# Optimization experiments

Hardware: AMD Instinct MI355X
Metric: run time of the kernel (lower is better)

The kernel has to match this reference:

```python
import jax, jax.numpy as jnp
import numpy as np

DIM = 64  # QK head dim, matches init kwarg 'dim'

def setup_inputs() -> dict:
    key = jax.random.key(0)
    kq, kk, kv = jax.random.split(key, 3)
    B, L, C, D, H = 2, 2048, 16, DIM, 64
    query = jax.random.normal(kq, (B, L, C, D), dtype=jnp.float32)
    k_ = jax.random.normal(kk, (B, L, C, D), dtype=jnp.float32)
    value = jax.random.normal(kv, (B, L, C, H), dtype=jnp.float32)
    return {"query": query, "key": k_, "value": value}

def reference(query, key, value):
    scaler = 1.0 / jnp.sqrt(jnp.float32(DIM))
    # score: [b, c, l, m]
    score = jnp.einsum('blcd,bmcd->bclm', query, key) * scaler
    # mask=False, dropout=0 -> identity
    attn = jax.nn.softmax(score, axis=3)
    # out: [b, l, c, h]
    out = jnp.einsum('bmch,bclm->blch', value, attn)
    return out
```

## Files before the change

### kernel.cpp

```cpp
#include <hip/hip_runtime.h>
#include <hip/hip_bf16.h>
#include <stdint.h>

#define B_ 2
#define L_ 2048
#define C_ 16
#define D_ 64
#define H_ 64
#define QBLK 128
#define KVBLK 64
#define NTILES 32
#define NTHREADS 256
#define NHEADS 32
#define TILE_ELEMS 4096
#define TENSOR_ELEMS (NHEADS * NTILES * TILE_ELEMS)

typedef __attribute__((ext_vector_type(8))) short bf16x8;
typedef __attribute__((ext_vector_type(16))) float f32x16;
typedef __attribute__((ext_vector_type(8))) unsigned short u16x8;

__device__ inline unsigned short f2bf(float f) {
  union { float f; unsigned int u; } v; v.f = f;
  unsigned int u = v.u;
  unsigned int r = (u + 0x7FFFu + ((u >> 16) & 1u)) >> 16;
  return (unsigned short)r;
}

__device__ inline float fast_exp2(float x) {
#if __has_builtin(__builtin_amdgcn_exp2f)
  return __builtin_amdgcn_exp2f(x);
#else
  return exp2f(x);
#endif
}

__device__ inline void gload_lds16(const unsigned short* g, unsigned short* l) {
  __builtin_amdgcn_global_load_lds(
      (const __attribute__((address_space(1))) unsigned int*)g,
      (__attribute__((address_space(3))) unsigned int*)l, 16, 0, 0);
}

__device__ inline unsigned cvt_pk_bf16(float lo, float hi) {
  unsigned r;
  asm("v_cvt_pk_bf16_f32 %0, %1, %2" : "=v"(r) : "v"(lo), "v"(hi));
  return r;
}

__device__ inline void pl32swap(unsigned &x, unsigned &y) {
#if __has_builtin(__builtin_amdgcn_permlane32_swap)
  auto r = __builtin_amdgcn_permlane32_swap(x, y, false, false);
  x = r[0]; y = r[1];
#else
  asm("v_permlane32_swap_b32 %0, %1" : "+v"(x), "+&v"(y));
#endif
}

__device__ inline float xmax32(float v) {
  unsigned x = __float_as_uint(v), y = x;
  pl32swap(x, y);
  return fmaxf(__uint_as_float(x), __uint_as_float(y));
}

__device__ inline float xsum32(float v) {
  unsigned x = __float_as_uint(v), y = x;
  pl32swap(x, y);
  return __uint_as_float(x) + __uint_as_float(y);
}

#define SLOT(grp, row) ((grp) ^ ((row) & 7) ^ (((row) & 8) >> 1))

__global__ __launch_bounds__(256) void prepack_kernel(
    const float* __restrict__ Kg, const float* __restrict__ Vg,
    unsigned short* __restrict__ Kb, unsigned short* __restrict__ Vb) {
  int idx = blockIdx.x * 256 + threadIdx.x;
  if (idx < 524288) {
    int i = idx;
    int grp = i & 7, row = (i >> 3) & 63, t = (i >> 9) & 31, head = i >> 14;
    int b = head >> 4, c = head & 15;
    const float* src = Kg + ((size_t)(b * L_ + t * 64 + row) * C_ + c) * D_ + grp * 8;
    float4 a0 = ((const float4*)src)[0];
    float4 a1 = ((const float4*)src)[1];
    u16x8 pk;
    pk[0] = f2bf(a0.x); pk[1] = f2bf(a0.y); pk[2] = f2bf(a0.z); pk[3] = f2bf(a0.w);
    pk[4] = f2bf(a1.x); pk[5] = f2bf(a1.y); pk[6] = f2bf(a1.z); pk[7] = f2bf(a1.w);
    size_t dst = ((size_t)(head * 32 + t) * 64 + row) * 64 + SLOT(grp, row) * 8;
    *(u16x8*)&Kb[dst] = pk;
  } else {
    int i = idx - 524288;
    int h = i & 63, grp = (i >> 6) & 7, t = (i >> 9) & 31, head = i >> 14;
    int b = head >> 4, c = head & 15;
    const float* src = Vg + ((size_t)(b * L_ + t * 64 + grp * 8) * C_ + c) * H_ + h;
    u16x8 pv;
#pragma unroll
    for (int j = 0; j < 8; ++j) pv[j] = f2bf(src[(size_t)j * C_ * H_]);
    size_t dst = ((size_t)(head * 32 + t) * 64 + h) * 64 + SLOT(grp, h) * 8;
    *(u16x8*)&Vb[dst] = pv;
  }
}

__global__ __launch_bounds__(NTHREADS, 2) void attn_fwd_kernel(
    const float* __restrict__ Qg,
    const unsigned short* __restrict__ Kb,
    const unsigned short* __restrict__ Vb,
    float* __restrict__ Og) {
  __shared__ unsigned short Ks2[3][TILE_ELEMS];
  __shared__ unsigned short Vt2[3][TILE_ELEMS];

  const int tid  = threadIdx.x;
  const int lane = tid & 63;
  const int w    = tid >> 6;
  const int ql   = lane & 31;
  const int u    = lane >> 5;

  const int bid   = blockIdx.x;
  const int swz   = (bid & 7) * 64 + (bid >> 3);
  const int head  = swz >> 4;
  const int qtile = swz & 15;
  const int b     = head >> 4;
  const int c     = head & 15;
  const int q0    = qtile * QBLK;

  const unsigned short* KbH = Kb + (size_t)head * NTILES * TILE_ELEMS;
  const unsigned short* VbH = Vb + (size_t)head * NTILES * TILE_ELEMS;

  const int qr = q0 + w * 32 + ql;
  const float* qrow = Qg + ((size_t)(b * L_ + qr) * C_ + c) * D_;
  bf16x8 qf[4];
#pragma unroll
  for (int ks = 0; ks < 4; ++ks) {
    float4 a0 = *(const float4*)(qrow + ks * 16 + u * 8);
    float4 a1 = *(const float4*)(qrow + ks * 16 + u * 8 + 4);
    bf16x8 q8;
    q8[0] = (short)f2bf(a0.x); q8[1] = (short)f2bf(a0.y);
    q8[2] = (short)f2bf(a0.z); q8[3] = (short)f2bf(a0.w);
    q8[4] = (short)f2bf(a1.x); q8[5] = (short)f2bf(a1.y);
    q8[6] = (short)f2bf(a1.z); q8[7] = (short)f2bf(a1.w);
    qf[ks] = q8;
  }

  f32x16 o0, o1;
#pragma unroll
  for (int i = 0; i < 16; ++i) { o0[i] = 0.f; o1[i] = 0.f; }
  float m_i = -1e30f, l_i = 0.f;
  const float sc2 = 0.125f * 1.44269504088896340736f;

  gload_lds16(KbH + tid * 8, &Ks2[0][tid * 8]);
  gload_lds16(KbH + 2048 + tid * 8, &Ks2[0][2048 + tid * 8]);
  gload_lds16(VbH + tid * 8, &Vt2[0][tid * 8]);
  gload_lds16(VbH + 2048 + tid * 8, &Vt2[0][2048 + tid * 8]);
  gload_lds16(KbH + TILE_ELEMS + tid * 8, &Ks2[1][tid * 8]);
  gload_lds16(KbH + TILE_ELEMS + 2048 + tid * 8, &Ks2[1][2048 + tid * 8]);
  gload_lds16(VbH + TILE_ELEMS + tid * 8, &Vt2[1][tid * 8]);
  gload_lds16(VbH + TILE_ELEMS + 2048 + tid * 8, &Vt2[1][2048 + tid * 8]);
  asm volatile("s_waitcnt vmcnt(4)" ::: "memory");
  __builtin_amdgcn_s_barrier();
  __builtin_amdgcn_sched_barrier(0);

  int cur = 0, stg = 2;
  for (int t = 0; t < NTILES; ++t) {
    {
      const int tl = (t + 2 < NTILES) ? (t + 2) : (NTILES - 1);
      const size_t toff = (size_t)tl * TILE_ELEMS + tid * 8;
      gload_lds16(KbH + toff, &Ks2[stg][tid * 8]);
      gload_lds16(KbH + toff + 2048, &Ks2[stg][2048 + tid * 8]);
      gload_lds16(VbH + toff, &Vt2[stg][tid * 8]);
      gload_lds16(VbH + toff + 2048, &Vt2[stg][2048 + tid * 8]);
    }

    const unsigned short* KsB = Ks2[cur];
    const unsigned short* VtB = Vt2[cur];

    f32x16 s0, s1;
#pragma unroll
    for (int i = 0; i < 16; ++i) { s0[i] = 0.f; s1[i] = 0.f; }
    __builtin_amdgcn_s_setprio(1);
#pragma unroll
    for (int ks = 0; ks < 4; ++ks) {
      const int col8 = 2 * ks + u;
      const int sw = SLOT(col8, ql) * 8;
      const bf16x8 ka0 = *(const bf16x8*)&KsB[ql * 64 + sw];
      const bf16x8 ka1 = *(const bf16x8*)&KsB[(32 + ql) * 64 + sw];
      s0 = __builtin_amdgcn_mfma_f32_32x32x16_bf16(ka0, qf[ks], s0, 0, 0, 0);
      s1 = __builtin_amdgcn_mfma_f32_32x32x16_bf16(ka1, qf[ks], s1, 0, 0, 0);
    }
    __builtin_amdgcn_s_setprio(0);

    float a8[8];
#pragma unroll
    for (int i = 0; i < 8; ++i)
      a8[i] = fmaxf(fmaxf(s0[i], s0[i + 8]), fmaxf(s1[i], s1[i + 8]));
    float b4a = fmaxf(a8[0], a8[1]), b4b = fmaxf(a8[2], a8[3]);
    float b4c = fmaxf(a8[4], a8[5]), b4d = fmaxf(a8[6], a8[7]);
    float rm = fmaxf(fmaxf(b4a, b4b), fmaxf(b4c, b4d));
    rm = xmax32(rm);
    const float rmx = rm * sc2;
    if (__any(rmx > m_i + 8.f)) {
      float mn = fmaxf(m_i, rmx);
      float so = fast_exp2(m_i - mn);
      m_i = mn;
#pragma unroll
      for (int i = 0; i < 16; ++i) { o0[i] *= so; o1[i] *= so; }
      l_i *= so;
    }

    float rst[4];
    bf16x8 pf[4];
#pragma unroll
    for (int tq = 0; tq < 4; ++tq) {
      const int be = ((2 * tq) & 3) * 4;
      const int bo = ((2 * tq + 1) & 3) * 4;
      float p0[4], p1[4];
#pragma unroll
      for (int r = 0; r < 4; ++r) {
        float se = (tq < 2) ? s0[be + r] : s1[be + r];
        float so_ = (tq < 2) ? s0[bo + r] : s1[bo + r];
        p0[r] = fast_exp2(__builtin_fmaf(se, sc2, -m_i));
        p1[r] = fast_exp2(__builtin_fmaf(so_, sc2, -m_i));
      }
      rst[tq] = ((p0[0] + p0[1]) + (p0[2] + p0[3])) +
                ((p1[0] + p1[1]) + (p1[2] + p1[3]));
      unsigned x0 = cvt_pk_bf16(p0[0], p0[1]);
      unsigned x1 = cvt_pk_bf16(p0[2], p0[3]);
      unsigned y0 = cvt_pk_bf16(p1[0], p1[1]);
      unsigned y1 = cvt_pk_bf16(p1[2], p1[3]);
      pl32swap(x0, y0);
      pl32swap(x1, y1);
      union { unsigned wd[4]; bf16x8 v; } pk;
      pk.wd[0] = x0; pk.wd[1] = x1; pk.wd[2] = y0; pk.wd[3] = y1;
      pf[tq] = pk.v;
    }
    l_i += xsum32((rst[0] + rst[1]) + (rst[2] + rst[3]));

    __builtin_amdgcn_s_setprio(1);
#pragma unroll
    for (int m = 0; m < 4; ++m) {
      const int col8 = 2 * m + u;
      const int sw = SLOT(col8, ql) * 8;
      const bf16x8 va0 = *(const bf16x8*)&VtB[ql * 64 + sw];
      const bf16x8 va1 = *(const bf16x8*)&VtB[(32 + ql) * 64 + sw];
      o0 = __builtin_amdgcn_mfma_f32_32x32x16_bf16(va0, pf[m], o0, 0, 0, 0);
      o1 = __builtin_amdgcn_mfma_f32_32x32x16_bf16(va1, pf[m], o1, 0, 0, 0);
    }
    __builtin_amdgcn_s_setprio(0);

    __builtin_amdgcn_sched_barrier(0);
    asm volatile("s_waitcnt vmcnt(4) lgkmcnt(0)" ::: "memory");
    __builtin_amdgcn_s_barrier();
    __builtin_amdgcn_sched_barrier(0);

    cur = (cur == 2) ? 0 : cur + 1;
    stg = (stg == 2) ? 0 : stg + 1;
  }

  const float inv = 1.0f / l_i;
  float* orow = Og + ((size_t)(b * L_ + qr) * C_ + c) * H_;
#pragma unroll
  for (int rg = 0; rg < 4; ++rg) {
    float4 v0, v1;
    v0.x = o0[rg * 4 + 0] * inv; v0.y = o0[rg * 4 + 1] * inv;
    v0.z = o0[rg * 4 + 2] * inv; v0.w = o0[rg * 4 + 3] * inv;
    v1.x = o1[rg * 4 + 0] * inv; v1.y = o1[rg * 4 + 1] * inv;
    v1.z = o1[rg * 4 + 2] * inv; v1.w = o1[rg * 4 + 3] * inv;
    *(float4*)(orow + 8 * rg + 4 * u) = v0;
    *(float4*)(orow + 32 + 8 * rg + 4 * u) = v1;
  }
}

extern "C" void kernel_launch(void* const* d_in, const int* in_sizes, int n_in,
                              void* d_out, int out_size, void* d_ws, size_t ws_size,
                              hipStream_t stream) {
  const float* Qg = (const float*)d_in[0];
  const float* Kg = (const float*)d_in[1];
  const float* Vg = (const float*)d_in[2];
  float* Og = (float*)d_out;

  unsigned short* Kb = (unsigned short*)d_ws;
  unsigned short* Vb = Kb + (size_t)TENSOR_ELEMS;

  prepack_kernel<<<4096, 256, 0, stream>>>(Kg, Vg, Kb, Vb);

  dim3 grid(NHEADS * (L_ / QBLK));
  dim3 block(NTHREADS);
  attn_fwd_kernel<<<grid, block, 0, stream>>>(Qg, Kb, Vb, Og);
}
```

Before: 69.04 us.

## Process two 32-row query groups per wave to double K/V tile reuse

Doubles the query block from 128 to 256 rows so that each wave handles two 32-row query groups. Each K and V fragment read from LDS feeds four MFMAs instead of two, and the grid halves to 256 blocks. This cuts K/V global and LDS traffic per query. In exchange, register pressure roughly doubles, so launch bounds drop to one block per SIMD group, and the smaller grid may underfill the 256 CUs.

```diff
diff --git a/kernel.cpp b/kernel.cpp
--- a/kernel.cpp
+++ b/kernel.cpp
@@ -7,7 +7,7 @@
 #define C_ 16
 #define D_ 64
 #define H_ 64
-#define QBLK 128
+#define QBLK 256
 #define KVBLK 64
 #define NTILES 32
 #define NTHREADS 256
@@ -98,7 +98,7 @@
   }
 }
 
-__global__ __launch_bounds__(NTHREADS, 2) void attn_fwd_kernel(
+__global__ __launch_bounds__(NTHREADS, 1) void attn_fwd_kernel(
     const float* __restrict__ Qg,
     const unsigned short* __restrict__ Kb,
     const unsigned short* __restrict__ Vb,
@@ -113,9 +113,9 @@
   const int u    = lane >> 5;
 
   const int bid   = blockIdx.x;
-  const int swz   = (bid & 7) * 64 + (bid >> 3);
-  const int head  = swz >> 4;
-  const int qtile = swz & 15;
+  const int swz   = (bid & 7) * 32 + (bid >> 3);
+  const int head  = swz >> 3;
+  const int qtile = swz & 7;
   const int b     = head >> 4;
   const int c     = head & 15;
   const int q0    = qtile * QBLK;
@@ -123,25 +123,33 @@
   const unsigned short* KbH = Kb + (size_t)head * NTILES * TILE_ELEMS;
   const unsigned short* VbH = Vb + (size_t)head * NTILES * TILE_ELEMS;
 
-  const int qr = q0 + w * 32 + ql;
-  const float* qrow = Qg + ((size_t)(b * L_ + qr) * C_ + c) * D_;
-  bf16x8 qf[4];
-#pragma unroll
-  for (int ks = 0; ks < 4; ++ks) {
-    float4 a0 = *(const float4*)(qrow + ks * 16 + u * 8);
-    float4 a1 = *(const float4*)(qrow + ks * 16 + u * 8 + 4);
-    bf16x8 q8;
-    q8[0] = (short)f2bf(a0.x); q8[1] = (short)f2bf(a0.y);
-    q8[2] = (short)f2bf(a0.z); q8[3] = (short)f2bf(a0.w);
-    q8[4] = (short)f2bf(a1.x); q8[5] = (short)f2bf(a1.y);
-    q8[6] = (short)f2bf(a1.z); q8[7] = (short)f2bf(a1.w);
-    qf[ks] = q8;
+  bf16x8 qf[2][4];
+#pragma unroll
+  for (int g = 0; g < 2; ++g) {
+    const int qr = q0 + w * 64 + g * 32 + ql;
+    const float* qrow = Qg + ((size_t)(b * L_ + qr) * C_ + c) * D_;
+#pragma unroll
+    for (int ks = 0; ks < 4; ++ks) {
+      float4 a0 = *(const float4*)(qrow + ks * 16 + u * 8);
+      float4 a1 = *(const float4*)(qrow + ks * 16 + u * 8 + 4);
+      bf16x8 q8;
+      q8[0] = (short)f2bf(a0.x); q8[1] = (short)f2bf(a0.y);
+      q8[2] = (short)f2bf(a0.z); q8[3] = (short)f2bf(a0.w);
+      q8[4] = (short)f2bf(a1.x); q8[5] = (short)f2bf(a1.y);
+      q8[6] = (short)f2bf(a1.z); q8[7] = (short)f2bf(a1.w);
+      qf[g][ks] = q8;
+    }
   }
 
-  f32x16 o0, o1;
-#pragma unroll
-  for (int i = 0; i < 16; ++i) { o0[i] = 0.f; o1[i] = 0.f; }
-  float m_i = -1e30f, l_i = 0.f;
+  f32x16 o[2][2];
+#pragma unroll
+  for (int g = 0; g < 2; ++g)
+#pragma unroll
+    for (int hb = 0; hb < 2; ++hb)
+#pragma unroll
+      for (int i = 0; i < 16; ++i) o[g][hb][i] = 0.f;
+  float m_i[2] = {-1e30f, -1e30f};
+  float l_i[2] = {0.f, 0.f};
   const float sc2 = 0.125f * 1.44269504088896340736f;
 
   gload_lds16(KbH + tid * 8, &Ks2[0][tid * 8]);
@@ -170,9 +178,13 @@
     const unsigned short* KsB = Ks2[cur];
     const unsigned short* VtB = Vt2[cur];
 
-    f32x16 s0, s1;
-#pragma unroll
-    for (int i = 0; i < 16; ++i) { s0[i] = 0.f; s1[i] = 0.f; }
+    f32x16 s[2][2];
+#pragma unroll
+    for (int g = 0; g < 2; ++g)
+#pragma unroll
+      for (int hf = 0; hf < 2; ++hf)
+#pragma unroll
+        for (int i = 0; i < 16; ++i) s[g][hf][i] = 0.f;
     __builtin_amdgcn_s_setprio(1);
 #pragma unroll
     for (int ks = 0; ks < 4; ++ks) {
@@ -180,56 +192,62 @@
       const int sw = SLOT(col8, ql) * 8;
       const bf16x8 ka0 = *(const bf16x8*)&KsB[ql * 64 + sw];
       const bf16x8 ka1 = *(const bf16x8*)&KsB[(32 + ql) * 64 + sw];
-      s0 = __builtin_amdgcn_mfma_f32_32x32x16_bf16(ka0, qf[ks], s0, 0, 0, 0);
-      s1 = __builtin_amdgcn_mfma_f32_32x32x16_bf16(ka1, qf[ks], s1, 0, 0, 0);
+      s[0][0] = __builtin_amdgcn_mfma_f32_32x32x16_bf16(ka0, qf[0][ks], s[0][0], 0, 0, 0);
+      s[0][1] = __builtin_amdgcn_mfma_f32_32x32x16_bf16(ka1, qf[0][ks], s[0][1], 0, 0, 0);
+      s[1][0] = __builtin_amdgcn_mfma_f32_32x32x16_bf16(ka0, qf[1][ks], s[1][0], 0, 0, 0);
+      s[1][1] = __builtin_amdgcn_mfma_f32_32x32x16_bf16(ka1, qf[1][ks], s[1][1], 0, 0, 0);
     }
     __builtin_amdgcn_s_setprio(0);
 
-    float a8[8];
-#pragma unroll
-    for (int i = 0; i < 8; ++i)
-      a8[i] = fmaxf(fmaxf(s0[i], s0[i + 8]), fmaxf(s1[i], s1[i + 8]));
-    float b4a = fmaxf(a8[0], a8[1]), b4b = fmaxf(a8[2], a8[3]);
-    float b4c = fmaxf(a8[4], a8[5]), b4d = fmaxf(a8[6], a8[7]);
-    float rm = fmaxf(fmaxf(b4a, b4b), fmaxf(b4c, b4d));
-    rm = xmax32(rm);
-    const float rmx = rm * sc2;
-    if (__any(rmx > m_i + 8.f)) {
-      float mn = fmaxf(m_i, rmx);
-      float so = fast_exp2(m_i - mn);
-      m_i = mn;
-#pragma unroll
-      for (int i = 0; i < 16; ++i) { o0[i] *= so; o1[i] *= so; }
-      l_i *= so;
-    }
-
-    float rst[4];
-    bf16x8 pf[4];
-#pragma unroll
-    for (int tq = 0; tq < 4; ++tq) {
-      const int be = ((2 * tq) & 3) * 4;
-      const int bo = ((2 * tq + 1) & 3) * 4;
-      float p0[4], p1[4];
-#pragma unroll
-      for (int r = 0; r < 4; ++r) {
-        float se = (tq < 2) ? s0[be + r] : s1[be + r];
-        float so_ = (tq < 2) ? s0[bo + r] : s1[bo + r];
-        p0[r] = fast_exp2(__builtin_fmaf(se, sc2, -m_i));
-        p1[r] = fast_exp2(__builtin_fmaf(so_, sc2, -m_i));
+    bf16x8 pf[2][4];
+#pragma unroll
+    for (int g = 0; g < 2; ++g) {
+      float a8[8];
+#pragma unroll
+      for (int i = 0; i < 8; ++i)
+        a8[i] = fmaxf(fmaxf(s[g][0][i], s[g][0][i + 8]),
+                      fmaxf(s[g][1][i], s[g][1][i + 8]));
+      float b4a = fmaxf(a8[0], a8[1]), b4b = fmaxf(a8[2], a8[3]);
+      float b4c = fmaxf(a8[4], a8[5]), b4d = fmaxf(a8[6], a8[7]);
+      float rm = fmaxf(fmaxf(b4a, b4b), fmaxf(b4c, b4d));
+      rm = xmax32(rm);
+      const float rmx = rm * sc2;
+      if (__any(rmx > m_i[g] + 8.f)) {
+        float mn = fmaxf(m_i[g], rmx);
+        float so = fast_exp2(m_i[g] - mn);
+        m_i[g] = mn;
+#pragma unroll
+        for (int i = 0; i < 16; ++i) { o[g][0][i] *= so; o[g][1][i] *= so; }
+        l_i[g] *= so;
       }
-      rst[tq] = ((p0[0] + p0[1]) + (p0[2] + p0[3])) +
-                ((p1[0] + p1[1]) + (p1[2] + p1[3]));
-      unsigned x0 = cvt_pk_bf16(p0[0], p0[1]);
-      unsigned x1 = cvt_pk_bf16(p0[2], p0[3]);
-      unsigned y0 = cvt_pk_bf16(p1[0], p1[1]);
-      unsigned y1 = cvt_pk_bf16(p1[2], p1[3]);
-      pl32swap(x0, y0);
-      pl32swap(x1, y1);
-      union { unsigned wd[4]; bf16x8 v; } pk;
-      pk.wd[0] = x0; pk.wd[1] = x1; pk.wd[2] = y0; pk.wd[3] = y1;
-      pf[tq] = pk.v;
-    }
-    l_i += xsum32((rst[0] + rst[1]) + (rst[2] + rst[3]));
+
+      float rst[4];
+#pragma unroll
+      for (int tq = 0; tq < 4; ++tq) {
+        const int be = ((2 * tq) & 3) * 4;
+        const int bo = ((2 * tq + 1) & 3) * 4;
+        float p0[4], p1[4];
+#pragma unroll
+        for (int r = 0; r < 4; ++r) {
+          float se = (tq < 2) ? s[g][0][be + r] : s[g][1][be + r];
+          float so_ = (tq < 2) ? s[g][0][bo + r] : s[g][1][bo + r];
+          p0[r] = fast_exp2(__builtin_fmaf(se, sc2, -m_i[g]));
+          p1[r] = fast_exp2(__builtin_fmaf(so_, sc2, -m_i[g]));
+        }
+        rst[tq] = ((p0[0] + p0[1]) + (p0[2] + p0[3])) +
+                  ((p1[0] + p1[1]) + (p1[2] + p1[3]));
+        unsigned x0 = cvt_pk_bf16(p0[0], p0[1]);
+        unsigned x1 = cvt_pk_bf16(p0[2], p0[3]);
+        unsigned y0 = cvt_pk_bf16(p1[0], p1[1]);
+        unsigned y1 = cvt_pk_bf16(p1[2], p1[3]);
+        pl32swap(x0, y0);
+        pl32swap(x1, y1);
+        union { unsigned wd[4]; bf16x8 v; } pk;
+        pk.wd[0] = x0; pk.wd[1] = x1; pk.wd[2] = y0; pk.wd[3] = y1;
+        pf[g][tq] = pk.v;
+      }
+      l_i[g] += xsum32((rst[0] + rst[1]) + (rst[2] + rst[3]));
+    }
 
     __builtin_amdgcn_s_setprio(1);
 #pragma unroll
@@ -238,8 +256,10 @@
       const int sw = SLOT(col8, ql) * 8;
       const bf16x8 va0 = *(const bf16x8*)&VtB[ql * 64 + sw];
       const bf16x8 va1 = *(const bf16x8*)&VtB[(32 + ql) * 64 + sw];
-      o0 = __builtin_amdgcn_mfma_f32_32x32x16_bf16(va0, pf[m], o0, 0, 0, 0);
-      o1 = __builtin_amdgcn_mfma_f32_32x32x16_bf16(va1, pf[m], o1, 0, 0, 0);
+      o[0][0] = __builtin_amdgcn_mfma_f32_32x32x16_bf16(va0, pf[0][m], o[0][0], 0, 0, 0);
+      o[0][1] = __builtin_amdgcn_mfma_f32_32x32x16_bf16(va1, pf[0][m], o[0][1], 0, 0, 0);
+      o[1][0] = __builtin_amdgcn_mfma_f32_32x32x16_bf16(va0, pf[1][m], o[1][0], 0, 0, 0);
+      o[1][1] = __builtin_amdgcn_mfma_f32_32x32x16_bf16(va1, pf[1][m], o[1][1], 0, 0, 0);
     }
     __builtin_amdgcn_s_setprio(0);
 
@@ -252,17 +272,21 @@
     stg = (stg == 2) ? 0 : stg + 1;
   }
 
-  const float inv = 1.0f / l_i;
-  float* orow = Og + ((size_t)(b * L_ + qr) * C_ + c) * H_;
-#pragma unroll
-  for (int rg = 0; rg < 4; ++rg) {
-    float4 v0, v1;
-    v0.x = o0[rg * 4 + 0] * inv; v0.y = o0[rg * 4 + 1] * inv;
-    v0.z = o0[rg * 4 + 2] * inv; v0.w = o0[rg * 4 + 3] * inv;
-    v1.x = o1[rg * 4 + 0] * inv; v1.y = o1[rg * 4 + 1] * inv;
-    v1.z = o1[rg * 4 + 2] * inv; v1.w = o1[rg * 4 + 3] * inv;
-    *(float4*)(orow + 8 * rg + 4 * u) = v0;
-    *(float4*)(orow + 32 + 8 * rg + 4 * u) = v1;
+#pragma unroll
+  for (int g = 0; g < 2; ++g) {
+    const float inv = 1.0f / l_i[g];
+    const int qr = q0 + w * 64 + g * 32 + ql;
+    float* orow = Og + ((size_t)(b * L_ + qr) * C_ + c) * H_;
+#pragma unroll
+    for (int rg = 0; rg < 4; ++rg) {
+      float4 v0, v1;
+      v0.x = o[g][0][rg * 4 + 0] * inv; v0.y = o[g][0][rg * 4 + 1] * inv;
+      v0.z = o[g][0][rg * 4 + 2] * inv; v0.w = o[g][0][rg * 4 + 3] * inv;
+      v1.x = o[g][1][rg * 4 + 0] * inv; v1.y = o[g][1][rg * 4 + 1] * inv;
+      v1.z = o[g][1][rg * 4 + 2] * inv; v1.w = o[g][1][rg * 4 + 3] * inv;
+      *(float4*)(orow + 8 * rg + 4 * u) = v0;
+      *(float4*)(orow + 32 + 8 * rg + 4 * u) = v1;
+    }
   }
 }
 
```

Result: slower. 82.74 us (+19.8%).

## Load K fragments directly into registers and drop K LDS staging

Applied to the files above, without the earlier changes.

The prepack kernel now lays K out in MFMA fragment order, so each lane can load its eight K operand vectors straight from global memory into registers, prefetched one tile ahead. K no longer passes through shared memory, and V drops from triple to double buffering, which frees LDS. The cost is that every wave reloads K from global or L2 independently instead of sharing one LDS copy, and registers rise by 8 bf16x8 prefetch vectors. The old fine-grained vmcnt waits are replaced by plain __syncthreads, which may expose more load latency each iteration.

```diff
diff --git a/kernel.cpp b/kernel.cpp
--- a/kernel.cpp
+++ b/kernel.cpp
@@ -75,15 +75,18 @@
   int idx = blockIdx.x * 256 + threadIdx.x;
   if (idx < 524288) {
     int i = idx;
-    int grp = i & 7, row = (i >> 3) & 63, t = (i >> 9) & 31, head = i >> 14;
+    int lane = i & 63, frag = (i >> 6) & 7, t = (i >> 9) & 31, head = i >> 14;
     int b = head >> 4, c = head & 15;
-    const float* src = Kg + ((size_t)(b * L_ + t * 64 + row) * C_ + c) * D_ + grp * 8;
+    int ks = frag >> 1, half = frag & 1;
+    int row = half * 32 + (lane & 31);
+    int kb = ks * 16 + (lane >> 5) * 8;
+    const float* src = Kg + ((size_t)(b * L_ + t * 64 + row) * C_ + c) * D_ + kb;
     float4 a0 = ((const float4*)src)[0];
     float4 a1 = ((const float4*)src)[1];
     u16x8 pk;
     pk[0] = f2bf(a0.x); pk[1] = f2bf(a0.y); pk[2] = f2bf(a0.z); pk[3] = f2bf(a0.w);
     pk[4] = f2bf(a1.x); pk[5] = f2bf(a1.y); pk[6] = f2bf(a1.z); pk[7] = f2bf(a1.w);
-    size_t dst = ((size_t)(head * 32 + t) * 64 + row) * 64 + SLOT(grp, row) * 8;
+    size_t dst = ((((size_t)(head * 32 + t)) * 8 + frag) * 64 + lane) * 8;
     *(u16x8*)&Kb[dst] = pk;
   } else {
     int i = idx - 524288;
@@ -103,8 +106,7 @@
     const unsigned short* __restrict__ Kb,
     const unsigned short* __restrict__ Vb,
     float* __restrict__ Og) {
-  __shared__ unsigned short Ks2[3][TILE_ELEMS];
-  __shared__ unsigned short Vt2[3][TILE_ELEMS];
+  __shared__ unsigned short Vt2[2][TILE_ELEMS];
 
   const int tid  = threadIdx.x;
   const int lane = tid & 63;
@@ -120,7 +122,7 @@
   const int c     = head & 15;
   const int q0    = qtile * QBLK;
 
-  const unsigned short* KbH = Kb + (size_t)head * NTILES * TILE_ELEMS;
+  const unsigned short* KbL = Kb + (size_t)head * NTILES * TILE_ELEMS + lane * 8;
   const unsigned short* VbH = Vb + (size_t)head * NTILES * TILE_ELEMS;
 
   const int qr = q0 + w * 32 + ql;
@@ -144,31 +146,26 @@
   float m_i = -1e30f, l_i = 0.f;
   const float sc2 = 0.125f * 1.44269504088896340736f;
 
-  gload_lds16(KbH + tid * 8, &Ks2[0][tid * 8]);
-  gload_lds16(KbH + 2048 + tid * 8, &Ks2[0][2048 + tid * 8]);
+  bf16x8 kfr[8];
+#pragma unroll
+  for (int f = 0; f < 8; ++f)
+    kfr[f] = *(const bf16x8*)(KbL + f * 512);
   gload_lds16(VbH + tid * 8, &Vt2[0][tid * 8]);
   gload_lds16(VbH + 2048 + tid * 8, &Vt2[0][2048 + tid * 8]);
-  gload_lds16(KbH + TILE_ELEMS + tid * 8, &Ks2[1][tid * 8]);
-  gload_lds16(KbH + TILE_ELEMS + 2048 + tid * 8, &Ks2[1][2048 + tid * 8]);
-  gload_lds16(VbH + TILE_ELEMS + tid * 8, &Vt2[1][tid * 8]);
-  gload_lds16(VbH + TILE_ELEMS + 2048 + tid * 8, &Vt2[1][2048 + tid * 8]);
-  asm volatile("s_waitcnt vmcnt(4)" ::: "memory");
-  __builtin_amdgcn_s_barrier();
-  __builtin_amdgcn_sched_barrier(0);
-
-  int cur = 0, stg = 2;
+  __syncthreads();
+
+  int cur = 0;
   for (int t = 0; t < NTILES; ++t) {
-    {
-      const int tl = (t + 2 < NTILES) ? (t + 2) : (NTILES - 1);
-      const size_t toff = (size_t)tl * TILE_ELEMS + tid * 8;
-      gload_lds16(KbH + toff, &Ks2[stg][tid * 8]);
-      gload_lds16(KbH + toff + 2048, &Ks2[stg][2048 + tid * 8]);
-      gload_lds16(VbH + toff, &Vt2[stg][tid * 8]);
-      gload_lds16(VbH + toff + 2048, &Vt2[stg][2048 + tid * 8]);
-    }
-
-    const unsigned short* KsB = Ks2[cur];
-    const unsigned short* VtB = Vt2[cur];
+    const int tl = (t + 1 < NTILES) ? (t + 1) : (NTILES - 1);
+    bf16x8 kn[8];
+#pragma unroll
+    for (int f = 0; f < 8; ++f)
+      kn[f] = *(const bf16x8*)(KbL + (size_t)(tl * 8 + f) * 512);
+    if (t + 1 < NTILES) {
+      const size_t toff = (size_t)(t + 1) * TILE_ELEMS + tid * 8;
+      gload_lds16(VbH + toff, &Vt2[cur ^ 1][tid * 8]);
+      gload_lds16(VbH + toff + 2048, &Vt2[cur ^ 1][2048 + tid * 8]);
+    }
 
     f32x16 s0, s1;
 #pragma unroll
@@ -176,12 +173,8 @@
     __builtin_amdgcn_s_setprio(1);
 #pragma unroll
     for (int ks = 0; ks < 4; ++ks) {
-      const int col8 = 2 * ks + u;
-      const int sw = SLOT(col8, ql) * 8;
-      const bf16x8 ka0 = *(const bf16x8*)&KsB[ql * 64 + sw];
-      const bf16x8 ka1 = *(const bf16x8*)&KsB[(32 + ql) * 64 + sw];
-      s0 = __builtin_amdgcn_mfma_f32_32x32x16_bf16(ka0, qf[ks], s0, 0, 0, 0);
-      s1 = __builtin_amdgcn_mfma_f32_32x32x16_bf16(ka1, qf[ks], s1, 0, 0, 0);
+      s0 = __builtin_amdgcn_mfma_f32_32x32x16_bf16(kfr[2 * ks], qf[ks], s0, 0, 0, 0);
+      s1 = __builtin_amdgcn_mfma_f32_32x32x16_bf16(kfr[2 * ks + 1], qf[ks], s1, 0, 0, 0);
     }
     __builtin_amdgcn_s_setprio(0);
 
@@ -231,6 +224,7 @@
     }
     l_i += xsum32((rst[0] + rst[1]) + (rst[2] + rst[3]));
 
+    const unsigned short* VtB = Vt2[cur];
     __builtin_amdgcn_s_setprio(1);
 #pragma unroll
     for (int m = 0; m < 4; ++m) {
@@ -243,13 +237,10 @@
     }
     __builtin_amdgcn_s_setprio(0);
 
-    __builtin_amdgcn_sched_barrier(0);
-    asm volatile("s_waitcnt vmcnt(4) lgkmcnt(0)" ::: "memory");
-    __builtin_amdgcn_s_barrier();
-    __builtin_amdgcn_sched_barrier(0);
-
-    cur = (cur == 2) ? 0 : cur + 1;
-    stg = (stg == 2) ? 0 : stg + 1;
+    __syncthreads();
+#pragma unroll
+    for (int f = 0; f < 8; ++f) kfr[f] = kn[f];
+    cur ^= 1;
   }
 
   const float inv = 1.0f / l_i;
```

Result: slower. 71.30 us (+3.3%).
